# Optimization experiments

Hardware: AMD Instinct MI355X
Metric: run time of the kernel (lower is better)

The kernel has to match this reference:

```python
import jax, jax.numpy as jnp
import numpy as np

B, N, D_IN, D_OUT = 8, 256, 128, 128


def setup_inputs() -> dict:
    key = jax.random.key(0)
    k1, k2, k3, k4, k5 = jax.random.split(key, 5)
    hidden = jax.random.normal(k1, (B, N, D_IN), dtype=jnp.float32)
    adj = jax.random.uniform(k2, (B, N, N), dtype=jnp.float32)
    dep_embed = jax.random.normal(k3, (B, N, N, D_IN), dtype=jnp.float32)
    weight = jax.random.normal(k4, (D_IN, D_OUT), dtype=jnp.float32) * 0.05
    bias_weight = jax.random.normal(k5, (D_OUT,), dtype=jnp.float32) * 0.05
    return {"hidden": hidden, "adj": adj, "dep_embed": dep_embed,
            "weight": weight, "bias_weight": bias_weight}


def reference(hidden, adj, dep_embed, weight, bias_weight):
    # fusion[b,p,q,d] = (hidden[b,p] + dep_embed[b,p,q]) @ W   (broadcast instead of tile)
    fusion = jnp.einsum('bpqe,ed->bpqd', hidden[:, :, None, :] + dep_embed, weight)
    # out[b,i,d] = sum_j adj[b,i,j] * fusion[b,j,i,d]   (transpose+mask+reduce fused)
    out = jnp.einsum('bij,bjid->bid', adj, fusion)
    return out + bias_weight
```

## Files before the change

kernel.cpp:

```cpp
#include <hip/hip_runtime.h>


constexpr int Bc  = 8;
constexpr int Nc  = 256;
constexpr int Dc  = 128;
constexpr int JC  = 16;
constexpr int NCH = Nc / JC;
constexpr int IT  = 32;
constexpr int NIQ = Nc / IT;

__global__ __launch_bounds__(256) void depgcn_k1(
    const float* __restrict__ hidden,
    const float* __restrict__ adj,
    const float* __restrict__ dep,
    float* __restrict__ P)
{
    const int blk = blockIdx.x;
    const int iq  = blk & (NIQ - 1);
    const int jc  = (blk >> 3) & (NCH - 1);
    const int b   = blk >> 7;
    const int t   = threadIdx.x;
    const int g   = t >> 5;
    const int c   = t & 31;

    __shared__ float sH[JC][Dc];
    __shared__ float sA[IT][JC];

    {
        const int row = t >> 4;
        const int col = (t & 15) * 8;
        const float* hp = hidden + ((size_t)b * Nc + jc * JC + row) * Dc + col;
        *(float4*)&sH[row][col]     = *(const float4*)hp;
        *(float4*)&sH[row][col + 4] = *(const float4*)(hp + 4);
    }
    {
        const int iL = t >> 3;
        const int jL = (t & 7) * 2;
        const float* ap = adj + ((size_t)b * Nc + iq * IT + iL) * Nc + jc * JC + jL;
        sA[iL][jL]     = ap[0];
        sA[iL][jL + 1] = ap[1];
    }
    __syncthreads();

    float4 acc[4];
    #pragma unroll
    for (int ii = 0; ii < 4; ++ii) acc[ii] = make_float4(0.f, 0.f, 0.f, 0.f);

    const float* depB = dep +
        ((((size_t)b * Nc + jc * JC) * Nc) + iq * IT + g * 4) * Dc + (size_t)c * 4;

    #pragma unroll 2
    for (int j = 0; j < JC; ++j) {
        const float4 h4 = *(const float4*)&sH[j][c * 4];
        const float* dj = depB + (size_t)j * Nc * Dc;
        #pragma unroll
        for (int ii = 0; ii < 4; ++ii) {
            const float  a  = sA[g * 4 + ii][j];
            const float4 d4 = *(const float4*)(dj + (size_t)ii * Dc);
            acc[ii].x = fmaf(a, d4.x + h4.x, acc[ii].x);
            acc[ii].y = fmaf(a, d4.y + h4.y, acc[ii].y);
            acc[ii].z = fmaf(a, d4.z + h4.z, acc[ii].z);
            acc[ii].w = fmaf(a, d4.w + h4.w, acc[ii].w);
        }
    }

    #pragma unroll
    for (int ii = 0; ii < 4; ++ii) {
        const int ig = iq * IT + g * 4 + ii;
        float* pp = P + (((size_t)b * Nc + ig) * NCH + jc) * Dc + (size_t)c * 4;
        *(float4*)pp = acc[ii];
    }
}

__global__ __launch_bounds__(256) void depgcn_k2(
    const float* __restrict__ P,
    const float* __restrict__ W,
    const float* __restrict__ bias,
    float* __restrict__ out)
{
    const int bi = blockIdx.x;
    const int b  = bi >> 8;
    const int i  = bi & (Nc - 1);
    const int t  = threadIdx.x;

    __shared__ float sT[Dc];
    __shared__ float sO[2][Dc];

    if (t < Dc) {
        const float* pp = P + ((size_t)b * Nc + i) * NCH * Dc + t;
        float s = 0.f;
        #pragma unroll
        for (int ch = 0; ch < NCH; ++ch) s += pp[(size_t)ch * Dc];
        sT[t] = s;
    }
    __syncthreads();

    {
        const int d = t & (Dc - 1);
        const int h = t >> 7;
        const float* wp = W + (size_t)(h * 64) * Dc + d;
        float s = 0.f;
        #pragma unroll 8
        for (int e = 0; e < 64; ++e)
            s = fmaf(sT[h * 64 + e], wp[(size_t)e * Dc], s);
        sO[h][d] = s;
    }
    __syncthreads();

    if (t < Dc) {
        out[((size_t)b * Nc + i) * Dc + t] = sO[0][t] + sO[1][t] + bias[t];
    }
}

extern "C" void kernel_launch(void* const* d_in, const int* in_sizes, int n_in,
                              void* d_out, int out_size, void* d_ws, size_t ws_size,
                              hipStream_t stream) {
    const float* hidden = (const float*)d_in[0];
    const float* adj    = (const float*)d_in[1];
    const float* dep    = (const float*)d_in[2];
    const float* W      = (const float*)d_in[3];
    const float* bias   = (const float*)d_in[4];
    float* out          = (float*)d_out;
    float* P            = (float*)d_ws;

    depgcn_k1<<<dim3(Bc * NCH * NIQ), dim3(256), 0, stream>>>(hidden, adj, dep, P);
    depgcn_k2<<<dim3(Bc * Nc), dim3(256), 0, stream>>>(P, W, bias, out);
}
```

Before: 374.2 us.

## Split hidden term out of dep reduction and shrink i-tile for more blocks

Uses linearity to separate the hidden contribution: the first kernel now reduces only adj-weighted dep_embed, and the second kernel adds sum_j adj[i,j]*hidden[j] (an adj@hidden product) before applying W. The i-tile is halved so the first kernel launches twice as many blocks, each thread handles two i rows and keeps its adj weights in registers, and the kernel has an occupancy hint. This drops the per-element add and the shared-memory hidden staging from the memory-bound dep stream, at the cost of a heavier second kernel that reads adj and hidden per output row.

```diff
diff --git a/kernel.cpp b/kernel.cpp
--- a/kernel.cpp
+++ b/kernel.cpp
@@ -6,74 +6,69 @@
 constexpr int Dc  = 128;
 constexpr int JC  = 16;
 constexpr int NCH = Nc / JC;
-constexpr int IT  = 32;
+constexpr int IT  = 16;
 constexpr int NIQ = Nc / IT;
 
-__global__ __launch_bounds__(256) void depgcn_k1(
-    const float* __restrict__ hidden,
+__global__ __launch_bounds__(256, 4) void depgcn_k1(
     const float* __restrict__ adj,
     const float* __restrict__ dep,
     float* __restrict__ P)
 {
     const int blk = blockIdx.x;
     const int iq  = blk & (NIQ - 1);
-    const int jc  = (blk >> 3) & (NCH - 1);
-    const int b   = blk >> 7;
+    const int jc  = (blk >> 4) & (NCH - 1);
+    const int b   = blk >> 8;
     const int t   = threadIdx.x;
     const int g   = t >> 5;
     const int c   = t & 31;
 
-    __shared__ float sH[JC][Dc];
     __shared__ float sA[IT][JC];
 
     {
-        const int row = t >> 4;
-        const int col = (t & 15) * 8;
-        const float* hp = hidden + ((size_t)b * Nc + jc * JC + row) * Dc + col;
-        *(float4*)&sH[row][col]     = *(const float4*)hp;
-        *(float4*)&sH[row][col + 4] = *(const float4*)(hp + 4);
-    }
-    {
-        const int iL = t >> 3;
-        const int jL = (t & 7) * 2;
-        const float* ap = adj + ((size_t)b * Nc + iq * IT + iL) * Nc + jc * JC + jL;
-        sA[iL][jL]     = ap[0];
-        sA[iL][jL + 1] = ap[1];
+        const int iL = t >> 4, jL = t & 15;
+        sA[iL][jL] = adj[((size_t)b * Nc + iq * IT + iL) * Nc + jc * JC + jL];
     }
     __syncthreads();
 
-    float4 acc[4];
+    float a0[JC], a1[JC];
     #pragma unroll
-    for (int ii = 0; ii < 4; ++ii) acc[ii] = make_float4(0.f, 0.f, 0.f, 0.f);
+    for (int j = 0; j < JC; ++j) { a0[j] = sA[g][j]; a1[j] = sA[g + 8][j]; }
 
-    const float* depB = dep +
-        ((((size_t)b * Nc + jc * JC) * Nc) + iq * IT + g * 4) * Dc + (size_t)c * 4;
+    const float* depB = dep + (((size_t)b * Nc + jc * JC) * Nc + iq * IT) * Dc
+                            + (size_t)c * 4;
 
-    #pragma unroll 2
+    float4 acc0 = make_float4(0.f, 0.f, 0.f, 0.f);
+    float4 acc1 = make_float4(0.f, 0.f, 0.f, 0.f);
+
+    #pragma unroll
     for (int j = 0; j < JC; ++j) {
-        const float4 h4 = *(const float4*)&sH[j][c * 4];
         const float* dj = depB + (size_t)j * Nc * Dc;
-        #pragma unroll
-        for (int ii = 0; ii < 4; ++ii) {
-            const float  a  = sA[g * 4 + ii][j];
-            const float4 d4 = *(const float4*)(dj + (size_t)ii * Dc);
-            acc[ii].x = fmaf(a, d4.x + h4.x, acc[ii].x);
-            acc[ii].y = fmaf(a, d4.y + h4.y, acc[ii].y);
-            acc[ii].z = fmaf(a, d4.z + h4.z, acc[ii].z);
-            acc[ii].w = fmaf(a, d4.w + h4.w, acc[ii].w);
-        }
+        const float4 d0 = *(const float4*)(dj + (size_t)g * Dc);
+        const float4 d1 = *(const float4*)(dj + (size_t)(g + 8) * Dc);
+        acc0.x = fmaf(a0[j], d0.x, acc0.x);
+        acc0.y = fmaf(a0[j], d0.y, acc0.y);
+        acc0.z = fmaf(a0[j], d0.z, acc0.z);
+        acc0.w = fmaf(a0[j], d0.w, acc0.w);
+        acc1.x = fmaf(a1[j], d1.x, acc1.x);
+        acc1.y = fmaf(a1[j], d1.y, acc1.y);
+        acc1.z = fmaf(a1[j], d1.z, acc1.z);
+        acc1.w = fmaf(a1[j], d1.w, acc1.w);
     }
 
-    #pragma unroll
-    for (int ii = 0; ii < 4; ++ii) {
-        const int ig = iq * IT + g * 4 + ii;
-        float* pp = P + (((size_t)b * Nc + ig) * NCH + jc) * Dc + (size_t)c * 4;
-        *(float4*)pp = acc[ii];
+    {
+        const int ig0 = iq * IT + g;
+        const int ig1 = ig0 + 8;
+        float* p0 = P + (((size_t)b * Nc + ig0) * NCH + jc) * Dc + (size_t)c * 4;
+        float* p1 = P + (((size_t)b * Nc + ig1) * NCH + jc) * Dc + (size_t)c * 4;
+        *(float4*)p0 = acc0;
+        *(float4*)p1 = acc1;
     }
 }
 
 __global__ __launch_bounds__(256) void depgcn_k2(
     const float* __restrict__ P,
+    const float* __restrict__ hidden,
+    const float* __restrict__ adj,
     const float* __restrict__ W,
     const float* __restrict__ bias,
     float* __restrict__ out)
@@ -82,34 +77,44 @@
     const int b  = bi >> 8;
     const int i  = bi & (Nc - 1);
     const int t  = threadIdx.x;
+    const int e  = t & (Dc - 1);
+    const int h  = t >> 7;
 
-    __shared__ float sT[Dc];
+    __shared__ float sAdj[Nc];
+    __shared__ float sTp[2][Dc];
     __shared__ float sO[2][Dc];
 
-    if (t < Dc) {
-        const float* pp = P + ((size_t)b * Nc + i) * NCH * Dc + t;
+    sAdj[t] = adj[((size_t)b * Nc + i) * Nc + t];
+    __syncthreads();
+
+    {
         float s = 0.f;
+        const float* pp = P + (((size_t)b * Nc + i) * NCH + h * 8) * Dc + e;
         #pragma unroll
-        for (int ch = 0; ch < NCH; ++ch) s += pp[(size_t)ch * Dc];
-        sT[t] = s;
+        for (int ch = 0; ch < 8; ++ch) s += pp[(size_t)ch * Dc];
+
+        const float* hp = hidden + ((size_t)b * Nc + h * 128) * Dc + e;
+        #pragma unroll 8
+        for (int jj = 0; jj < 128; ++jj)
+            s = fmaf(sAdj[h * 128 + jj], hp[(size_t)jj * Dc], s);
+        sTp[h][e] = s;
     }
     __syncthreads();
 
     {
-        const int d = t & (Dc - 1);
-        const int h = t >> 7;
-        const float* wp = W + (size_t)(h * 64) * Dc + d;
+        const float* wp = W + (size_t)(h * 64) * Dc + e;
         float s = 0.f;
         #pragma unroll 8
-        for (int e = 0; e < 64; ++e)
-            s = fmaf(sT[h * 64 + e], wp[(size_t)e * Dc], s);
-        sO[h][d] = s;
+        for (int q = 0; q < 64; ++q) {
+            const float te = sTp[0][h * 64 + q] + sTp[1][h * 64 + q];
+            s = fmaf(te, wp[(size_t)q * Dc], s);
+        }
+        sO[h][e] = s;
     }
     __syncthreads();
 
-    if (t < Dc) {
+    if (t < Dc)
         out[((size_t)b * Nc + i) * Dc + t] = sO[0][t] + sO[1][t] + bias[t];
-    }
 }
 
 extern "C" void kernel_launch(void* const* d_in, const int* in_sizes, int n_in,
@@ -123,6 +128,6 @@
     float* out          = (float*)d_out;
     float* P            = (float*)d_ws;
 
-    depgcn_k1<<<dim3(Bc * NCH * NIQ), dim3(256), 0, stream>>>(hidden, adj, dep, P);
-    depgcn_k2<<<dim3(Bc * Nc), dim3(256), 0, stream>>>(P, W, bias, out);
+    depgcn_k1<<<dim3(Bc * NCH * NIQ), dim3(256), 0, stream>>>(adj, dep, P);
+    depgcn_k2<<<dim3(Bc * Nc), dim3(256), 0, stream>>>(P, hidden, adj, W, bias, out);
 }
```

Result: slower. 399.9 us (+6.9%).
